# Kernel optimization log

Hardware: AMD Instinct MI355X
Metric: run time of the kernel (lower is better)

Reference implementation:

```python
import jax, jax.numpy as jnp
import numpy as np
from jax import lax

N_ITERS = 32     # fixed iteration count (random graph diameter << 32, converges)
NEG = -1e9       # finite stand-in for -inf so grads stay finite


def _seg_logsumexp(x, seg, n):
    # numerically stable log-sum-exp scatter over segments (per-node over out-edges)
    m = jax.ops.segment_max(x, seg, num_segments=n)
    m = jnp.maximum(m, NEG)  # empty segments give -inf -> floor at NEG
    s = jax.ops.segment_sum(jnp.exp(x - m[seg]), seg, num_segments=n)
    return jnp.where(s > 0, jnp.log(s) + m, NEG)


def setup_inputs() -> dict:
    key = jax.random.key(0)
    k1, k2 = jax.random.split(key)
    N, E, F = 50000, 1600000, 64
    # scaled uniform features -> edge utilities ~ -7.4 mean => contraction, VI converges
    feats = jax.random.uniform(k1, (E, F), dtype=jnp.float32) * 0.2
    edge_index = jax.random.randint(k2, (2, E), 0, N)
    dest_mask = (jnp.arange(N) % 100) == 0  # 500 destination nodes
    batch = jnp.zeros((N,), dtype=jnp.int32)  # single graph (unused by VI solver)
    weight = jnp.full((1, F), -1.0, dtype=jnp.float32)  # module's constant init
    bias = jnp.full((1,), -1.0, dtype=jnp.float32)
    return {"feats": feats, "dest_mask": dest_mask, "edge_index": edge_index,
            "batch": batch, "n_nodes": N, "weight": weight, "bias": bias}


def reference(feats, dest_mask, edge_index, batch, n_nodes, weight, bias):
    # util = clamp(Linear(feats), -100, -1e-6), shape [E, 1]
    util = jnp.clip(feats @ weight.T + bias, -100.0, -1e-6)
    u = util[:, 0]                      # [E]
    src, dst = edge_index[0], edge_index[1]

    # value iteration: V(i) = LSE_{e: src(e)=i} (u_e + V(dst_e)), V(dest) = 0
    v0 = jnp.where(dest_mask, 0.0, NEG)

    def step(v, _):
        v_new = _seg_logsumexp(u + v[dst], src, n_nodes)
        v_new = jnp.where(dest_mask, 0.0, v_new)
        return v_new, None

    value, _ = lax.scan(step, v0, None, length=N_ITERS)  # [N]

    # edge choice probability: P(e) = exp(u_e + V(dst_e) - V(src_e))
    prob = jnp.exp(u + value[dst] - value[src])          # [E]
    return value, util, prob
```

## Files before the change

kernel.cpp:

```cpp
#include <hip/hip_runtime.h>

#define NEGV (-1000000000.0f)
#define N_ITERS 32
#define NBUCK 512
#define B1 256
#define REG 4096
#define CPAD 16

__global__ __launch_bounds__(256) void util_kernel64gs(
    const float* __restrict__ feats, const float* __restrict__ weight,
    const float* __restrict__ bias, float* __restrict__ u,
    int* __restrict__ cursors, int* __restrict__ flags, int E)
{
    if (blockIdx.x == 0) {
        for (int i = threadIdx.x; i < NBUCK; i += 256)
            cursors[(size_t)i * CPAD] = i * REG;
        if (threadIdx.x <= N_ITERS)
            flags[threadIdx.x] = (threadIdx.x == 0) ? 1 : 0;
    }
    int tid = blockIdx.x * blockDim.x + threadIdx.x;
    int l = tid & 15;
    int g = tid >> 4;
    int ngroups = (gridDim.x * blockDim.x) >> 4;
    float4 wv = *reinterpret_cast<const float4*>(weight + l * 4);
    float bb = bias[0];
    for (int e = g; e < E; e += ngroups) {
        float4 fv = *reinterpret_cast<const float4*>(feats + (size_t)e * 64 + l * 4);
        float s = fv.x * wv.x + fv.y * wv.y + fv.z * wv.z + fv.w * wv.w;
        s += __shfl_xor(s, 8, 16);
        s += __shfl_xor(s, 4, 16);
        s += __shfl_xor(s, 2, 16);
        s += __shfl_xor(s, 1, 16);
        if (l == 0)
            u[e] = fminf(fmaxf(s + bb, -100.0f), -1e-6f);
    }
}

__global__ __launch_bounds__(256) void util_kernel(
    const float* __restrict__ feats, const float* __restrict__ weight,
    const float* __restrict__ bias, float* __restrict__ u,
    int* __restrict__ cursors, int* __restrict__ flags, int E, int F)
{
    if (blockIdx.x == 0) {
        for (int i = threadIdx.x; i < NBUCK; i += 256)
            cursors[(size_t)i * CPAD] = i * REG;
        if (threadIdx.x <= N_ITERS)
            flags[threadIdx.x] = (threadIdx.x == 0) ? 1 : 0;
    }
    int e = blockIdx.x * blockDim.x + threadIdx.x;
    if (e >= E) return;
    const float* row = feats + (size_t)e * (size_t)F;
    float acc = 0.0f;
    for (int f = 0; f < F; f += 4) {
        float4 fv = *reinterpret_cast<const float4*>(row + f);
        acc += fv.x * weight[f + 0];
        acc += fv.y * weight[f + 1];
        acc += fv.z * weight[f + 2];
        acc += fv.w * weight[f + 3];
    }
    acc += bias[0];
    u[e] = fminf(fmaxf(acc, -100.0f), -1e-6f);
}

__global__ __launch_bounds__(256) void scatter_fused(
    const int* __restrict__ src, const int* __restrict__ dst,
    const float* __restrict__ u, int* __restrict__ cursors,
    int2* __restrict__ edg, int E, int W, int chunk)
{
    __shared__ int h[NBUCK];
    for (int i = threadIdx.x; i < NBUCK; i += 256) h[i] = 0;
    __syncthreads();
    const int lo = blockIdx.x * chunk;
    const int hi = min(E, lo + chunk);
    for (int e = lo + threadIdx.x; e < hi; e += 256)
        atomicAdd(&h[(unsigned)src[e] / (unsigned)W], 1);
    __syncthreads();
    for (int k = threadIdx.x; k < NBUCK; k += 256) {
        int c = h[k];
        h[k] = (c > 0) ? atomicAdd(&cursors[(size_t)k * CPAD], c) : 0;
    }
    __syncthreads();
    for (int e = lo + threadIdx.x; e < hi; e += 256) {
        int s = src[e];
        unsigned k = (unsigned)s / (unsigned)W;
        int pos = atomicAdd(&h[k], 1);
        if (pos < (int)((k + 1) * REG)) {
            unsigned sl = (unsigned)s - k * (unsigned)W;
            int2 rec;
            rec.x = (int)((sl << 20) | (unsigned)dst[e]);
            rec.y = __float_as_int(expf(u[e]));
            edg[pos] = rec;
        }
    }
}

__global__ __launch_bounds__(256) void fine_sort(
    const int* __restrict__ cursors, int2* __restrict__ edg,
    int* __restrict__ row_ptr, int* __restrict__ row_end,
    const int* __restrict__ dest_mask, float* __restrict__ ew0,
    int N, int W)
{
    __shared__ int pks[REG];
    __shared__ int ubs[REG];
    __shared__ int fh[132];

    const int k  = blockIdx.x;
    const int lo = k * W;
    const int nn = min(N, lo + W) - lo;
    if (nn <= 0) return;

    for (int i = threadIdx.x; i < nn; i += 256)
        ew0[lo + i] = dest_mask[lo + i] ? 1.0f : 0.0f;

    const int bs = k * REG;
    int cnt = cursors[(size_t)k * CPAD] - bs;
    if (cnt > REG) cnt = REG;
    if (cnt < 0) cnt = 0;

    for (int i = threadIdx.x; i < cnt; i += 256) {
        int2 r = edg[bs + i];
        pks[i] = r.x;
        ubs[i] = r.y;
    }
    for (int i = threadIdx.x; i < nn; i += 256) fh[i] = 0;
    __syncthreads();

    for (int i = threadIdx.x; i < cnt; i += 256)
        atomicAdd(&fh[((unsigned)pks[i]) >> 20], 1);
    __syncthreads();

    if (threadIdx.x == 0) {
        int run = bs;
        for (int i = 0; i < nn; ++i) {
            int c = fh[i];
            fh[i] = run;
            row_ptr[lo + i] = run;
            row_end[lo + i] = run + c;
            run += c;
        }
    }
    __syncthreads();

    for (int i = threadIdx.x; i < cnt; i += 256) {
        int w = pks[i];
        int pos = atomicAdd(&fh[((unsigned)w) >> 20], 1);
        int2 r;
        r.x = w & 0xFFFFF;
        r.y = ubs[i];
        edg[pos] = r;
    }
}

__global__ __launch_bounds__(256) void iter_exp_conv(
    const int* __restrict__ row_ptr, const int* __restrict__ row_end,
    const int2* __restrict__ edg, const int* __restrict__ dest_mask,
    const float* __restrict__ ew, float* __restrict__ ew_new,
    const int* __restrict__ flag_prev, const int* __restrict__ flag_prev2,
    int* __restrict__ flag_cur, int N)
{
    __shared__ int blk_changed;
    int tid = blockIdx.x * blockDim.x + threadIdx.x;

    if (*flag_prev == 0) {
        if (*flag_prev2 == 0) return;
        if (tid < N) ew_new[tid] = ew[tid];
        return;
    }

    if (threadIdx.x == 0) blk_changed = 0;
    __syncthreads();

    int n = tid >> 3;
    int lane8 = tid & 7;
    if (n < N) {
        int rs = row_ptr[n];
        int re = row_end[n];
        float s = 0.0f;
        for (int j = rs + lane8; j < re; j += 8) {
            int2 r = edg[j];
            s += __int_as_float(r.y) * ew[r.x];
        }
        s += __shfl_xor(s, 4, 8);
        s += __shfl_xor(s, 2, 8);
        s += __shfl_xor(s, 1, 8);
        if (lane8 == 0) {
            float nv = dest_mask[n] ? 1.0f : s;
            ew_new[n] = nv;
            if (__float_as_int(nv) != __float_as_int(ew[n])) blk_changed = 1;
        }
    }
    __syncthreads();
    if (threadIdx.x == 0 && blk_changed) atomicOr(flag_cur, 1);
}

__global__ __launch_bounds__(256) void final_exp_conv(
    const int* __restrict__ row_ptr, const int* __restrict__ row_end,
    const int2* __restrict__ edg, const int* __restrict__ dest_mask,
    const float* __restrict__ ew, float* __restrict__ value,
    const int* __restrict__ flag_prev, int N)
{
    int tid = blockIdx.x * blockDim.x + threadIdx.x;

    if (*flag_prev == 0) {
        if (tid < N) {
            float s = ew[tid];
            value[tid] = dest_mask[tid] ? 0.0f : (s > 0.0f ? logf(s) : NEGV);
        }
        return;
    }

    int n = tid >> 3;
    int lane8 = tid & 7;
    if (n >= N) return;
    int rs = row_ptr[n];
    int re = row_end[n];
    float s = 0.0f;
    for (int j = rs + lane8; j < re; j += 8) {
        int2 r = edg[j];
        s += __int_as_float(r.y) * ew[r.x];
    }
    s += __shfl_xor(s, 4, 8);
    s += __shfl_xor(s, 2, 8);
    s += __shfl_xor(s, 1, 8);
    if (lane8 == 0)
        value[n] = dest_mask[n] ? 0.0f : (s > 0.0f ? logf(s) : NEGV);
}

__global__ __launch_bounds__(256) void prob_kernel(
    const float* __restrict__ u, const int* __restrict__ src,
    const int* __restrict__ dst, const float* __restrict__ v,
    float* __restrict__ prob, int E)
{
    int e = blockIdx.x * blockDim.x + threadIdx.x;
    if (e >= E) return;
    prob[e] = expf((u[e] + v[dst[e]]) - v[src[e]]);
}

__global__ __launch_bounds__(256) void util_plain(
    const float* __restrict__ feats, const float* __restrict__ weight,
    const float* __restrict__ bias, float* __restrict__ u, int E, int F)
{
    int e = blockIdx.x * blockDim.x + threadIdx.x;
    if (e >= E) return;
    const float* row = feats + (size_t)e * (size_t)F;
    float acc = 0.0f;
    for (int f = 0; f < F; f += 4) {
        float4 fv = *reinterpret_cast<const float4*>(row + f);
        acc += fv.x * weight[f + 0];
        acc += fv.y * weight[f + 1];
        acc += fv.z * weight[f + 2];
        acc += fv.w * weight[f + 3];
    }
    acc += bias[0];
    u[e] = fminf(fmaxf(acc, -100.0f), -1e-6f);
}
__global__ __launch_bounds__(256) void init_pass(
    const int* __restrict__ dest_mask, float* v, float* s, int N)
{
    int n = blockIdx.x * blockDim.x + threadIdx.x;
    if (n >= N) return;
    v[n] = dest_mask[n] ? 0.0f : NEGV;
    s[n] = 0.0f;
}
__global__ __launch_bounds__(256) void edge_pass(
    const float* __restrict__ u, const int* __restrict__ src,
    const int* __restrict__ dst, const float* __restrict__ v, float* s, int E)
{
    int e = blockIdx.x * blockDim.x + threadIdx.x;
    if (e >= E) return;
    atomicAdd(&s[src[e]], expf(u[e] + v[dst[e]]));
}
__global__ __launch_bounds__(256) void node_pass(
    const int* __restrict__ dest_mask, float* v, float* s, int N)
{
    int n = blockIdx.x * blockDim.x + threadIdx.x;
    if (n >= N) return;
    float sv = s[n];
    v[n] = dest_mask[n] ? 0.0f : (sv > 0.0f ? logf(sv) : NEGV);
    s[n] = 0.0f;
}

extern "C" void kernel_launch(void* const* d_in, const int* in_sizes, int n_in,
                              void* d_out, int out_size, void* d_ws, size_t ws_size,
                              hipStream_t stream)
{
    const float* feats     = (const float*)d_in[0];
    const int*   dest_mask = (const int*)d_in[1];
    const int*   edge_index= (const int*)d_in[2];
    const float* weight    = (const float*)d_in[5];
    const float* bias      = (const float*)d_in[6];

    const int F = in_sizes[5];
    const int E = in_sizes[2] / 2;
    const int N = in_sizes[1];

    const int* src = edge_index;
    const int* dst = edge_index + E;

    float* out   = (float*)d_out;
    float* value = out;
    float* util  = out + N;
    float* prob  = out + (size_t)N + (size_t)E;

    const int eb = (E + 255) / 256;
    const int nb = (N + 255) / 256;

    const int W = (N + NBUCK - 1) / NBUCK;

    const size_t need_words = (size_t)NBUCK * CPAD + 2 * (size_t)NBUCK * REG
                            + 4 * (size_t)N + (N_ITERS + 1);
    const size_t need_bytes = need_words * 4;
    const bool pack_ok = (N < (1 << 20)) && (W <= 128)
                      && ((size_t)NBUCK * REG >= (size_t)E);

    if (d_ws != nullptr && ws_size >= need_bytes && pack_ok) {
        int*   cursors = (int*)d_ws;
        int2*  edg     = (int2*)(cursors + (size_t)NBUCK * CPAD);
        int*   row_ptr = (int*)(edg + (size_t)NBUCK * REG);
        int*   row_end = row_ptr + N;
        float* ewa     = (float*)(row_end + N);
        float* ewb     = ewa + N;
        int*   flags   = (int*)(ewb + N);

        if (F == 64) {
            util_kernel64gs<<<2048, 256, 0, stream>>>(
                feats, weight, bias, util, cursors, flags, E);
        } else {
            util_kernel<<<eb, 256, 0, stream>>>(
                feats, weight, bias, util, cursors, flags, E, F);
        }

        const int chunk = (E + B1 - 1) / B1;
        scatter_fused<<<B1, 256, 0, stream>>>(src, dst, util, cursors, edg, E, W, chunk);
        fine_sort<<<NBUCK, 256, 0, stream>>>(
            cursors, edg, row_ptr, row_end, dest_mask, ewa, N, W);

        const int gb = ((N * 8) + 255) / 256;
        float* cur = ewa;
        float* nxt = ewb;
        for (int it = 1; it <= N_ITERS - 1; ++it) {
            const int* fp  = flags + (it - 1);
            const int* fp2 = flags + ((it >= 2) ? (it - 2) : 0);
            iter_exp_conv<<<gb, 256, 0, stream>>>(
                row_ptr, row_end, edg, dest_mask, cur, nxt, fp, fp2, flags + it, N);
            float* t = cur; cur = nxt; nxt = t;
        }
        final_exp_conv<<<gb, 256, 0, stream>>>(
            row_ptr, row_end, edg, dest_mask, cur, value, flags + (N_ITERS - 1), N);

        prob_kernel<<<eb, 256, 0, stream>>>(util, src, dst, value, prob, E);
    } else {
        util_plain<<<eb, 256, 0, stream>>>(feats, weight, bias, util, E, F);
        float* s = prob;
        init_pass<<<nb, 256, 0, stream>>>(dest_mask, value, s, N);
        for (int it = 0; it < N_ITERS; ++it) {
            edge_pass<<<eb, 256, 0, stream>>>(util, src, dst, value, s, E);
            node_pass<<<nb, 256, 0, stream>>>(dest_mask, value, s, N);
        }
        prob_kernel<<<eb, 256, 0, stream>>>(util, src, dst, value, prob, E);
    }
}
```

Baseline: 401.8 us.

## Fold first value-iteration step into fine_sort and use nontemporal feature loads

The first exp-space iteration moves into the tail of fine_sort, which now computes ew1 from the dest mask directly on the freshly sorted edge segments, and the launch loop starts at iteration 2. One launch of iter_exp_conv is saved. The flag reads become a single int2 load, which requires N to be even. Feature loads in the util kernel become nontemporal to avoid polluting cache with streamed data. The fused step runs within fine_sort's 512 blocks and does scattered reads of dest_mask.

```diff
diff --git a/kernel.cpp b/kernel.cpp
--- a/kernel.cpp
+++ b/kernel.cpp
@@ -7,6 +7,8 @@
 #define REG 4096
 #define CPAD 16
 
+typedef float f32x4 __attribute__((ext_vector_type(4)));
+
 __global__ __launch_bounds__(256) void util_kernel64gs(
     const float* __restrict__ feats, const float* __restrict__ weight,
     const float* __restrict__ bias, float* __restrict__ u,
@@ -16,16 +18,17 @@
         for (int i = threadIdx.x; i < NBUCK; i += 256)
             cursors[(size_t)i * CPAD] = i * REG;
         if (threadIdx.x <= N_ITERS)
-            flags[threadIdx.x] = (threadIdx.x == 0) ? 1 : 0;
+            flags[threadIdx.x] = (threadIdx.x <= 1) ? 1 : 0;
     }
     int tid = blockIdx.x * blockDim.x + threadIdx.x;
     int l = tid & 15;
     int g = tid >> 4;
     int ngroups = (gridDim.x * blockDim.x) >> 4;
-    float4 wv = *reinterpret_cast<const float4*>(weight + l * 4);
+    f32x4 wv = *reinterpret_cast<const f32x4*>(weight + l * 4);
     float bb = bias[0];
     for (int e = g; e < E; e += ngroups) {
-        float4 fv = *reinterpret_cast<const float4*>(feats + (size_t)e * 64 + l * 4);
+        f32x4 fv = __builtin_nontemporal_load(
+            reinterpret_cast<const f32x4*>(feats + (size_t)e * 64 + l * 4));
         float s = fv.x * wv.x + fv.y * wv.y + fv.z * wv.z + fv.w * wv.w;
         s += __shfl_xor(s, 8, 16);
         s += __shfl_xor(s, 4, 16);
@@ -45,7 +48,7 @@
         for (int i = threadIdx.x; i < NBUCK; i += 256)
             cursors[(size_t)i * CPAD] = i * REG;
         if (threadIdx.x <= N_ITERS)
-            flags[threadIdx.x] = (threadIdx.x == 0) ? 1 : 0;
+            flags[threadIdx.x] = (threadIdx.x <= 1) ? 1 : 0;
     }
     int e = blockIdx.x * blockDim.x + threadIdx.x;
     if (e >= E) return;
@@ -97,20 +100,18 @@
 __global__ __launch_bounds__(256) void fine_sort(
     const int* __restrict__ cursors, int2* __restrict__ edg,
     int* __restrict__ row_ptr, int* __restrict__ row_end,
-    const int* __restrict__ dest_mask, float* __restrict__ ew0,
+    const int* __restrict__ dest_mask, float* __restrict__ ew1,
     int N, int W)
 {
     __shared__ int pks[REG];
     __shared__ int ubs[REG];
     __shared__ int fh[132];
+    __shared__ int rst[132];
 
     const int k  = blockIdx.x;
     const int lo = k * W;
     const int nn = min(N, lo + W) - lo;
     if (nn <= 0) return;
-
-    for (int i = threadIdx.x; i < nn; i += 256)
-        ew0[lo + i] = dest_mask[lo + i] ? 1.0f : 0.0f;
 
     const int bs = k * REG;
     int cnt = cursors[(size_t)k * CPAD] - bs;
@@ -134,6 +135,7 @@
         for (int i = 0; i < nn; ++i) {
             int c = fh[i];
             fh[i] = run;
+            rst[i] = run;
             row_ptr[lo + i] = run;
             row_end[lo + i] = run + c;
             run += c;
@@ -149,20 +151,42 @@
         r.y = ubs[i];
         edg[pos] = r;
     }
+    __syncthreads();
+
+    const int grp   = threadIdx.x >> 3;
+    const int lane8 = threadIdx.x & 7;
+    for (int base = 0; base < nn; base += 32) {
+        int ridx = base + grp;
+        if (ridx < nn) {
+            int n  = lo + ridx;
+            int rs = rst[ridx];
+            int re = fh[ridx];
+            float s = 0.0f;
+            for (int j = rs + lane8; j < re; j += 8) {
+                int2 r = edg[j];
+                s += __int_as_float(r.y) * (dest_mask[r.x] ? 1.0f : 0.0f);
+            }
+            s += __shfl_xor(s, 4, 8);
+            s += __shfl_xor(s, 2, 8);
+            s += __shfl_xor(s, 1, 8);
+            if (lane8 == 0)
+                ew1[n] = dest_mask[n] ? 1.0f : s;
+        }
+    }
 }
 
 __global__ __launch_bounds__(256) void iter_exp_conv(
     const int* __restrict__ row_ptr, const int* __restrict__ row_end,
     const int2* __restrict__ edg, const int* __restrict__ dest_mask,
     const float* __restrict__ ew, float* __restrict__ ew_new,
-    const int* __restrict__ flag_prev, const int* __restrict__ flag_prev2,
-    int* __restrict__ flag_cur, int N)
+    const int* __restrict__ flag_prev2, int* __restrict__ flag_cur, int N)
 {
     __shared__ int blk_changed;
     int tid = blockIdx.x * blockDim.x + threadIdx.x;
 
-    if (*flag_prev == 0) {
-        if (*flag_prev2 == 0) return;
+    int2 fl = *reinterpret_cast<const int2*>(flag_prev2);
+    if (fl.y == 0) {
+        if (fl.x == 0) return;
         if (tid < N) ew_new[tid] = ew[tid];
         return;
     }
@@ -311,7 +335,8 @@
                             + 4 * (size_t)N + (N_ITERS + 1);
     const size_t need_bytes = need_words * 4;
     const bool pack_ok = (N < (1 << 20)) && (W <= 128)
-                      && ((size_t)NBUCK * REG >= (size_t)E);
+                      && ((size_t)NBUCK * REG >= (size_t)E)
+                      && ((N & 1) == 0);
 
     if (d_ws != nullptr && ws_size >= need_bytes && pack_ok) {
         int*   cursors = (int*)d_ws;
@@ -338,11 +363,10 @@
         const int gb = ((N * 8) + 255) / 256;
         float* cur = ewa;
         float* nxt = ewb;
-        for (int it = 1; it <= N_ITERS - 1; ++it) {
-            const int* fp  = flags + (it - 1);
-            const int* fp2 = flags + ((it >= 2) ? (it - 2) : 0);
+        for (int it = 2; it <= N_ITERS - 1; ++it) {
             iter_exp_conv<<<gb, 256, 0, stream>>>(
-                row_ptr, row_end, edg, dest_mask, cur, nxt, fp, fp2, flags + it, N);
+                row_ptr, row_end, edg, dest_mask, cur, nxt,
+                flags + (it - 2), flags + it, N);
             float* t = cur; cur = nxt; nxt = t;
         }
         final_exp_conv<<<gb, 256, 0, stream>>>(
```

Result: faster. 361.6 us (-10.0%).
